# Optimization experiments

Measured on AMD Instinct MI355X. Metric: run time of the kernel, lower is better.

Reference implementation:

```python
import jax, jax.numpy as jnp
import numpy as np

NEIGHBOR_NUM = 4


def reference(vertices, feature_map, sample_idx):
    # vertices: (bs, n, 3), feature_map: (bs, n, c), sample_idx: (pool_num,)
    # pairwise squared distances: ||a||^2 + ||b||^2 - 2 a.b
    inner = jnp.einsum('bnd,bmd->bnm', vertices, vertices)  # (bs, n, n)
    quad = jnp.sum(vertices * vertices, axis=2)             # (bs, n)
    distance = -2.0 * inner + quad[:, None, :] + quad[:, :, None]
    # k+1 smallest distances (self is nearest); lax.top_k finds largest, so negate
    _, neighbor_index = jax.lax.top_k(-distance, NEIGHBOR_NUM + 1)
    neighbor_index = neighbor_index[:, :, 1:]               # drop self -> (bs, n, k)
    # gather neighbor features per batch: (bs, n, k, c)
    neighbor_feature = jax.vmap(lambda f, idx: f[idx])(feature_map, neighbor_index)
    pooled_feature = jnp.max(neighbor_feature, axis=2)      # (bs, n, c)
    vertices_pool = vertices[:, sample_idx, :]              # (bs, pool_num, 3)
    feature_map_pool = pooled_feature[:, sample_idx, :]     # (bs, pool_num, c)
    return vertices_pool, feature_map_pool


def setup_inputs() -> dict:
    key = jax.random.key(0)
    k1, k2 = jax.random.split(key)
    bs, n, c = 8, 4096, 256
    pool_num = n // 4
    vertices = jax.random.normal(k1, (bs, n, 3), dtype=jnp.float32)
    feature_map = jax.random.normal(k2, (bs, n, c), dtype=jnp.float32)
    sample_idx = jnp.arange(pool_num, dtype=jnp.int32)
    return {"vertices": vertices, "feature_map": feature_map, "sample_idx": sample_idx}
```

## Files before the change

kernel.cpp:

```cpp
#include <hip/hip_runtime.h>
#include <stdint.h>

#define BATCH 8
#define NPTS  4096
#define CH    256
#define QN    1024
#define WAVES_PER_BLOCK 16
#define BLOCK (WAVES_PER_BLOCK * 64)
#define BLOCKS_PER_BATCH (QN / WAVES_PER_BLOCK)

__device__ __forceinline__ float fmul(float a, float b) { return __fmul_rn(a, b); }
__device__ __forceinline__ float fadd(float a, float b) { return __fadd_rn(a, b); }

__device__ __forceinline__ void cswap(uint64_t& lo, uint64_t& hi) {
  uint64_t mn = hi < lo ? hi : lo;
  uint64_t mx = hi < lo ? lo : hi;
  lo = mn; hi = mx;
}

__global__ __launch_bounds__(BLOCK) void knn_pool_kernel(
    const float* __restrict__ verts,
    const float* __restrict__ feat,
    const int*   __restrict__ sidx,
    float* __restrict__ outV,
    float* __restrict__ outF)
{
  extern __shared__ float4 sv[];

  const int batch = blockIdx.x / BLOCKS_PER_BATCH;
  const int qblk  = blockIdx.x % BLOCKS_PER_BATCH;
  const float* vb = verts + (size_t)batch * (NPTS * 3);

  for (int c = threadIdx.x; c < NPTS; c += BLOCK) {
    float x = vb[c * 3 + 0];
    float y = vb[c * 3 + 1];
    float z = vb[c * 3 + 2];
    float q = fadd(fadd(fmul(x, x), fmul(y, y)), fmul(z, z));
    sv[c] = make_float4(x, y, z, q);
  }
  __syncthreads();

  const int wave = threadIdx.x >> 6;
  const int lane = threadIdx.x & 63;
  const int i = qblk * WAVES_PER_BLOCK + wave;
  const int n = sidx[i];
  const float4 vq = sv[n];

  uint64_t a0 = ~0ull, a1 = ~0ull, a2 = ~0ull, a3 = ~0ull, a4 = ~0ull;
#pragma unroll 8
  for (int c = lane; c < NPTS; c += 64) {
    float4 v = sv[c];
    float dot = fadd(fadd(fmul(vq.x, v.x), fmul(vq.y, v.y)), fmul(vq.z, v.z));
    float d = fadd(fadd(fmul(-2.0f, dot), v.w), vq.w);
    uint32_t bb = __float_as_uint(d);
    bb ^= (uint32_t)((int32_t)bb >> 31) | 0x80000000u;
    uint64_t key = ((uint64_t)bb << 32) | (uint32_t)c;
    a4 = key < a4 ? key : a4;
    cswap(a3, a4);
    cswap(a2, a3);
    cswap(a1, a2);
    cswap(a0, a1);
  }

  uint64_t prev = 0;
  uint64_t nb1, nb2, nb3, nb4;
#pragma unroll
  for (int r = 0; r < 5; ++r) {
    uint64_t cand = a0 > prev ? a0
                  : a1 > prev ? a1
                  : a2 > prev ? a2
                  : a3 > prev ? a3
                  : a4 > prev ? a4 : ~0ull;
#pragma unroll
    for (int s = 32; s >= 1; s >>= 1) {
      uint64_t o = (uint64_t)__shfl_xor((long long)cand, s, 64);
      if (o < cand) cand = o;
    }
    if (r == 1) nb1 = cand;
    if (r == 2) nb2 = cand;
    if (r == 3) nb3 = cand;
    if (r == 4) nb4 = cand;
    prev = cand;
  }

  const int n1 = (int)(uint32_t)nb1;
  const int n2 = (int)(uint32_t)nb2;
  const int n3 = (int)(uint32_t)nb3;
  const int n4 = (int)(uint32_t)nb4;

  const float* fb = feat + (size_t)batch * NPTS * CH;
  const int col = lane * 4;
  float4 f1 = *(const float4*)(fb + (size_t)n1 * CH + col);
  float4 f2 = *(const float4*)(fb + (size_t)n2 * CH + col);
  float4 f3 = *(const float4*)(fb + (size_t)n3 * CH + col);
  float4 f4 = *(const float4*)(fb + (size_t)n4 * CH + col);
  float4 r;
  r.x = fmaxf(fmaxf(f1.x, f2.x), fmaxf(f3.x, f4.x));
  r.y = fmaxf(fmaxf(f1.y, f2.y), fmaxf(f3.y, f4.y));
  r.z = fmaxf(fmaxf(f1.z, f2.z), fmaxf(f3.z, f4.z));
  r.w = fmaxf(fmaxf(f1.w, f2.w), fmaxf(f3.w, f4.w));
  *(float4*)(outF + ((size_t)batch * QN + i) * CH + col) = r;

  if (lane < 3) {
    outV[((size_t)batch * QN + i) * 3 + lane] = vb[(size_t)n * 3 + lane];
  }
}

extern "C" void kernel_launch(void* const* d_in, const int* in_sizes, int n_in,
                              void* d_out, int out_size, void* d_ws, size_t ws_size,
                              hipStream_t stream) {
  const float* verts = (const float*)d_in[0];
  const float* feat  = (const float*)d_in[1];
  const int*   sidx  = (const int*)d_in[2];
  float* outV = (float*)d_out;
  float* outF = (float*)d_out + (size_t)BATCH * QN * 3;

  dim3 grid(BATCH * BLOCKS_PER_BATCH);
  dim3 block(BLOCK);
  size_t lds_bytes = (size_t)NPTS * sizeof(float4);
  knn_pool_kernel<<<grid, block, lds_bytes, stream>>>(verts, feat, sidx, outV, outF);
}
```

Measured before the change: 42.39 us.

## Use per-lane top-2 fast path with exact top-5 fallback on overflow

The main scan now keeps only the two smallest keys per lane instead of five, which cuts the compare-swap chain and the registers held in the hot loop. After the wave-wide merge it checks whether any lane's second-best key is below the fifth global candidate, meaning that lane might have held more true neighbours than it kept. If so, the whole wave rescans with the full top-5 insertion, so results stay exact. The launch bounds also request more resident blocks. The fallback repeats the full distance pass, and with 64 candidates per lane and random points it may fire fairly often.

```diff
diff --git a/kernel.cpp b/kernel.cpp
--- a/kernel.cpp
+++ b/kernel.cpp
@@ -18,7 +18,18 @@
   lo = mn; hi = mx;
 }
 
-__global__ __launch_bounds__(BLOCK) void knn_pool_kernel(
+__device__ __forceinline__ float cdist(const float4 vq, const float4 v) {
+  float dot = fadd(fadd(fmul(vq.x, v.x), fmul(vq.y, v.y)), fmul(vq.z, v.z));
+  return fadd(fadd(fmul(-2.0f, dot), v.w), vq.w);
+}
+
+__device__ __forceinline__ uint64_t mkkey(float d, int c) {
+  uint32_t bb = __float_as_uint(d);
+  bb ^= (uint32_t)((int32_t)bb >> 31) | 0x80000000u;
+  return ((uint64_t)bb << 32) | (uint32_t)c;
+}
+
+__global__ __launch_bounds__(BLOCK, 8) void knn_pool_kernel(
     const float* __restrict__ verts,
     const float* __restrict__ feat,
     const int*   __restrict__ sidx,
@@ -45,32 +56,22 @@
   const int i = qblk * WAVES_PER_BLOCK + wave;
   const int n = sidx[i];
   const float4 vq = sv[n];
+  const float4* svp = sv + lane;
 
-  uint64_t a0 = ~0ull, a1 = ~0ull, a2 = ~0ull, a3 = ~0ull, a4 = ~0ull;
+  uint64_t a0 = ~0ull, a1 = ~0ull;
 #pragma unroll 8
-  for (int c = lane; c < NPTS; c += 64) {
-    float4 v = sv[c];
-    float dot = fadd(fadd(fmul(vq.x, v.x), fmul(vq.y, v.y)), fmul(vq.z, v.z));
-    float d = fadd(fadd(fmul(-2.0f, dot), v.w), vq.w);
-    uint32_t bb = __float_as_uint(d);
-    bb ^= (uint32_t)((int32_t)bb >> 31) | 0x80000000u;
-    uint64_t key = ((uint64_t)bb << 32) | (uint32_t)c;
-    a4 = key < a4 ? key : a4;
-    cswap(a3, a4);
-    cswap(a2, a3);
-    cswap(a1, a2);
+  for (int t = 0; t < NPTS / 64; ++t) {
+    float4 v = svp[t * 64];
+    uint64_t key = mkkey(cdist(vq, v), lane + t * 64);
+    a1 = key < a1 ? key : a1;
     cswap(a0, a1);
   }
 
   uint64_t prev = 0;
-  uint64_t nb1, nb2, nb3, nb4;
+  uint64_t nb1 = 0, nb2 = 0, nb3 = 0, nb4 = 0;
 #pragma unroll
   for (int r = 0; r < 5; ++r) {
-    uint64_t cand = a0 > prev ? a0
-                  : a1 > prev ? a1
-                  : a2 > prev ? a2
-                  : a3 > prev ? a3
-                  : a4 > prev ? a4 : ~0ull;
+    uint64_t cand = a0 > prev ? a0 : (a1 > prev ? a1 : ~0ull);
 #pragma unroll
     for (int s = 32; s >= 1; s >>= 1) {
       uint64_t o = (uint64_t)__shfl_xor((long long)cand, s, 64);
@@ -81,6 +82,39 @@
     if (r == 3) nb3 = cand;
     if (r == 4) nb4 = cand;
     prev = cand;
+  }
+
+  bool bad = (a1 < nb4);
+  if (__any(bad)) {
+    uint64_t b0 = ~0ull, b1 = ~0ull, b2 = ~0ull, b3 = ~0ull, b4 = ~0ull;
+    for (int t = 0; t < NPTS / 64; ++t) {
+      float4 v = svp[t * 64];
+      uint64_t key = mkkey(cdist(vq, v), lane + t * 64);
+      b4 = key < b4 ? key : b4;
+      cswap(b3, b4);
+      cswap(b2, b3);
+      cswap(b1, b2);
+      cswap(b0, b1);
+    }
+    prev = 0;
+#pragma unroll
+    for (int r = 0; r < 5; ++r) {
+      uint64_t cand = b0 > prev ? b0
+                    : b1 > prev ? b1
+                    : b2 > prev ? b2
+                    : b3 > prev ? b3
+                    : b4 > prev ? b4 : ~0ull;
+#pragma unroll
+      for (int s = 32; s >= 1; s >>= 1) {
+        uint64_t o = (uint64_t)__shfl_xor((long long)cand, s, 64);
+        if (o < cand) cand = o;
+      }
+      if (r == 1) nb1 = cand;
+      if (r == 2) nb2 = cand;
+      if (r == 3) nb3 = cand;
+      if (r == 4) nb4 = cand;
+      prev = cand;
+    }
   }
 
   const int n1 = (int)(uint32_t)nb1;
```

Result: slower. 44.19 us (+4.2%).
